# Kernel optimization log

Hardware: AMD Instinct MI355X
Metric: run time of the kernel (lower is better)

The kernel has to match this reference:

```python
import jax, jax.numpy as jnp
import numpy as np
from itertools import product


def _unnormalize(g, size, align_corners=True):
    # map [-1,1] -> pixel coords
    if align_corners:
        return (g + 1.0) * 0.5 * (size - 1)
    return ((g + 1.0) * size - 1.0) * 0.5


def grid_sample_4d(inp, grid, align_corners=True, padding_mode='zeros'):
    """inp: [N,C,X,Y,U,V], grid: [N,P,4] in [-1,1] -> out [N,C,P].
    16-corner quadrilinear interpolation."""
    N, C, X, Y, U, V = inp.shape
    sizes = (X, Y, U, V)
    coords = [_unnormalize(grid[..., d], sizes[d], align_corners) for d in range(4)]
    if padding_mode == 'border':
        coords = [jnp.clip(c, 0.0, sizes[d] - 1) for d, c in enumerate(coords)]
    lo = [jnp.floor(c) for c in coords]                     # [N,P] each
    frac = [c - l for c, l in zip(coords, lo)]
    lo_i = [l.astype(jnp.int32) for l in lo]
    inp_flat = inp.reshape(N, C, X * Y * U * V)
    out = jnp.zeros((N, C, grid.shape[1]), inp.dtype)
    for bits in product((0, 1), repeat=4):                  # 16 corners
        w = jnp.ones_like(frac[0])
        valid = jnp.ones(frac[0].shape, bool)
        idx = []
        for d in range(4):
            i = lo_i[d] + bits[d]
            w = w * (frac[d] if bits[d] else (1.0 - frac[d]))
            if padding_mode == 'zeros':
                valid = valid & (i >= 0) & (i < sizes[d])
            idx.append(jnp.clip(i, 0, sizes[d] - 1))
        if padding_mode == 'zeros':
            w = w * valid.astype(w.dtype)
        flat = ((idx[0] * Y + idx[1]) * U + idx[2]) * V + idx[3]   # [N,P]
        vals = jnp.take_along_axis(inp_flat, flat[:, None, :], axis=2)  # [N,C,P]
        out = out + w[:, None, :] * vals
    return out


def setup_inputs() -> dict:
    key = jax.random.key(0)
    k1, k2 = jax.random.split(key)
    N, C, X, Y, U, V = 1, 16, 8, 8, 256, 256
    P = 1_000_000
    inp = jax.random.normal(k1, (N, C, X, Y, U, V), dtype=jnp.float32)
    # slightly exceed [-1,1] to exercise zeros padding
    grid = jax.random.uniform(k2, (N, P, 4), dtype=jnp.float32, minval=-1.05, maxval=1.05)
    return {"input": inp, "grid": grid}


def reference(input, grid):
    return grid_sample_4d(input, grid, align_corners=True, padding_mode='zeros')
```

## Files before the change

### kernel.cpp

```cpp
#include <hip/hip_runtime.h>
#include <hip/hip_fp16.h>

namespace {
constexpr int CS = 16;
constexpr int XS = 8, YS = 8, US = 256, VS = 256;
constexpr int CH_STRIDE = XS * YS * US * VS;
constexpr size_t NVOX = (size_t)CH_STRIDE;
constexpr size_t TRANS_H_BYTES = NVOX * CS * 2;

__global__ __launch_bounds__(256) void transpose_h_kernel(
    const float* __restrict__ inp, __half* __restrict__ ws)
{
    __shared__ float lds[CS][257];
    size_t base = (size_t)blockIdx.x * 256;
    #pragma unroll
    for (int c = 0; c < CS; ++c)
        lds[c][threadIdx.x] = inp[(size_t)c * CH_STRIDE + base + threadIdx.x];
    __syncthreads();
    size_t obase = base * CS;
    #pragma unroll
    for (int it = 0; it < 2; ++it) {
        int flat0 = (it * 256 + threadIdx.x) * 8;
        uint4 pk;
        uint* pw = &pk.x;
        #pragma unroll
        for (int j = 0; j < 4; ++j) {
            int f0 = flat0 + j * 2, f1 = f0 + 1;
            __half2 h = __floats2half2_rn(lds[f0 & 15][f0 >> 4],
                                          lds[f1 & 15][f1 >> 4]);
            pw[j] = *reinterpret_cast<uint*>(&h);
        }
        *reinterpret_cast<uint4*>(ws + obase + flat0) = pk;
    }
}

__global__ __launch_bounds__(256) void gather_h_kernel(
    const __half* __restrict__ tin, const float* __restrict__ grid,
    float* __restrict__ out, int P)
{
    int p = blockIdx.x * 256 + threadIdx.x;
    if (p >= P) return;

    float4 g = reinterpret_cast<const float4*>(grid)[p];

    float c0 = (g.x + 1.0f) * 0.5f * (XS - 1);
    float c1 = (g.y + 1.0f) * 0.5f * (YS - 1);
    float c2 = (g.z + 1.0f) * 0.5f * (US - 1);
    float c3 = (g.w + 1.0f) * 0.5f * (VS - 1);

    float f0 = floorf(c0), f1 = floorf(c1), f2 = floorf(c2), f3 = floorf(c3);
    int i0 = (int)f0, i1 = (int)f1, i2 = (int)f2, i3 = (int)f3;
    float t0 = c0 - f0, t1 = c1 - f1, t2 = c2 - f2, t3 = c3 - f3;

    float w0[2], w1[2], w2[2], w3[2];
    int   q0[2], q1[2], q2[2], q3[2];
    #pragma unroll
    for (int b = 0; b < 2; ++b) {
        int j;
        j = i0 + b; w0[b] = (b ? t0 : 1.0f - t0) * ((j >= 0 && j < XS) ? 1.0f : 0.0f); q0[b] = min(max(j, 0), XS - 1);
        j = i1 + b; w1[b] = (b ? t1 : 1.0f - t1) * ((j >= 0 && j < YS) ? 1.0f : 0.0f); q1[b] = min(max(j, 0), YS - 1);
        j = i2 + b; w2[b] = (b ? t2 : 1.0f - t2) * ((j >= 0 && j < US) ? 1.0f : 0.0f); q2[b] = min(max(j, 0), US - 1);
        j = i3 + b; w3[b] = (b ? t3 : 1.0f - t3) * ((j >= 0 && j < VS) ? 1.0f : 0.0f); q3[b] = min(max(j, 0), VS - 1);
    }

    float a[16];
    #pragma unroll
    for (int i = 0; i < 16; ++i) a[i] = 0.0f;

    #pragma unroll
    for (int bx = 0; bx < 2; ++bx)
    #pragma unroll
    for (int by = 0; by < 2; ++by) {
        int   xy  = (q0[bx] * YS + q1[by]) << 16;
        float wxy = w0[bx] * w1[by];
        #pragma unroll
        for (int bu = 0; bu < 2; ++bu) {
            int   xyu  = xy + (q2[bu] << 8);
            float wxyu = wxy * w2[bu];
            #pragma unroll
            for (int bv = 0; bv < 2; ++bv) {
                int   vox = xyu + q3[bv];
                float w   = wxyu * w3[bv];
                const uint4* cp = reinterpret_cast<const uint4*>(tin) + (size_t)vox * 2;
                uint4 r0 = cp[0], r1 = cp[1];
                uint rr[8] = {r0.x, r0.y, r0.z, r0.w, r1.x, r1.y, r1.z, r1.w};
                #pragma unroll
                for (int j = 0; j < 8; ++j) {
                    float2 f = __half22float2(*reinterpret_cast<const __half2*>(&rr[j]));
                    a[2*j]     = fmaf(w, f.x, a[2*j]);
                    a[2*j + 1] = fmaf(w, f.y, a[2*j + 1]);
                }
            }
        }
    }

    #pragma unroll
    for (int c = 0; c < CS; ++c)
        __builtin_nontemporal_store(a[c], &out[(size_t)c * P + p]);
}

__global__ __launch_bounds__(256) void gs4d_fallback(
    const float* __restrict__ inp, const float* __restrict__ grid,
    float* __restrict__ out, int P)
{
    int p = blockIdx.x * 256 + threadIdx.x;
    if (p >= P) return;
    int c = blockIdx.y;
    float4 g = reinterpret_cast<const float4*>(grid)[p];
    float c0 = (g.x + 1.0f) * 0.5f * (XS - 1);
    float c1 = (g.y + 1.0f) * 0.5f * (YS - 1);
    float c2 = (g.z + 1.0f) * 0.5f * (US - 1);
    float c3 = (g.w + 1.0f) * 0.5f * (VS - 1);
    float f0 = floorf(c0), f1 = floorf(c1), f2 = floorf(c2), f3 = floorf(c3);
    int i0 = (int)f0, i1 = (int)f1, i2 = (int)f2, i3 = (int)f3;
    float t0 = c0 - f0, t1 = c1 - f1, t2 = c2 - f2, t3 = c3 - f3;
    float w0[2], w1[2], w2[2], w3[2];
    int   q0[2], q1[2], q2[2], q3[2];
    #pragma unroll
    for (int b = 0; b < 2; ++b) {
        int j;
        j = i0 + b; w0[b] = (b ? t0 : 1.0f - t0) * ((j >= 0 && j < XS) ? 1.0f : 0.0f); q0[b] = min(max(j, 0), XS - 1);
        j = i1 + b; w1[b] = (b ? t1 : 1.0f - t1) * ((j >= 0 && j < YS) ? 1.0f : 0.0f); q1[b] = min(max(j, 0), YS - 1);
        j = i2 + b; w2[b] = (b ? t2 : 1.0f - t2) * ((j >= 0 && j < US) ? 1.0f : 0.0f); q2[b] = min(max(j, 0), US - 1);
        j = i3 + b; w3[b] = (b ? t3 : 1.0f - t3) * ((j >= 0 && j < VS) ? 1.0f : 0.0f); q3[b] = min(max(j, 0), VS - 1);
    }
    const float* ip = inp + (size_t)c * CH_STRIDE;
    float acc = 0.0f;
    #pragma unroll
    for (int bx = 0; bx < 2; ++bx)
    #pragma unroll
    for (int by = 0; by < 2; ++by)
    #pragma unroll
    for (int bu = 0; bu < 2; ++bu)
    #pragma unroll
    for (int bv = 0; bv < 2; ++bv) {
        int idx = ((q0[bx] * YS + q1[by]) * US + q2[bu]) * VS + q3[bv];
        acc = fmaf(w0[bx] * w1[by] * w2[bu] * w3[bv], ip[idx], acc);
    }
    __builtin_nontemporal_store(acc, &out[(size_t)c * P + p]);
}
}

extern "C" void kernel_launch(void* const* d_in, const int* in_sizes, int n_in,
                              void* d_out, int out_size, void* d_ws, size_t ws_size,
                              hipStream_t stream) {
    const float* inp  = (const float*)d_in[0];
    const float* grid = (const float*)d_in[1];
    float* out = (float*)d_out;
    int P = in_sizes[1] / 4;
    int pblocks = (P + 255) / 256;

    if (ws_size >= TRANS_H_BYTES) {
        __half* ws = (__half*)d_ws;
        transpose_h_kernel<<<CH_STRIDE / 256, 256, 0, stream>>>(inp, ws);
        gather_h_kernel<<<pblocks, 256, 0, stream>>>(ws, grid, out, P);
    } else {
        dim3 blocks(pblocks, CS);
        gs4d_fallback<<<blocks, 256, 0, stream>>>(inp, grid, out, P);
    }
}
```

Baseline: 266.2 us.

## Add a second fp16 atlas shifted by one voxel to align v-neighbor pairs

The transpose kernel now writes two channel-interleaved fp16 copies of the input. The second copy is rotated by one voxel along V within each 256-voxel row. The gather kernel picks the copy by the parity of the lower V index, so the two V-neighbor voxels always start at an even slot and stay in one aligned 64-byte chunk, reducing cache-line crossings per gather. In exchange, the transpose writes twice as many bytes and the workspace footprint doubles, which may lower cache hit rates.

```diff
diff --git a/kernel.cpp b/kernel.cpp
--- a/kernel.cpp
+++ b/kernel.cpp
@@ -6,10 +6,12 @@
 constexpr int XS = 8, YS = 8, US = 256, VS = 256;
 constexpr int CH_STRIDE = XS * YS * US * VS;
 constexpr size_t NVOX = (size_t)CH_STRIDE;
-constexpr size_t TRANS_H_BYTES = NVOX * CS * 2;
-
-__global__ __launch_bounds__(256) void transpose_h_kernel(
-    const float* __restrict__ inp, __half* __restrict__ ws)
+constexpr size_t ATLAS_HALFS = NVOX * CS;
+constexpr size_t DUAL_BYTES  = ATLAS_HALFS * 2 * 2;
+constexpr size_t SINGLE_BYTES = ATLAS_HALFS * 2;
+
+__global__ __launch_bounds__(256) void transpose2_kernel(
+    const float* __restrict__ inp, __half* __restrict__ wsA, __half* __restrict__ wsB)
 {
     __shared__ float lds[CS][257];
     size_t base = (size_t)blockIdx.x * 256;
@@ -30,13 +32,14 @@
                                           lds[f1 & 15][f1 >> 4]);
             pw[j] = *reinterpret_cast<uint*>(&h);
         }
-        *reinterpret_cast<uint4*>(ws + obase + flat0) = pk;
-    }
-}
-
-__global__ __launch_bounds__(256) void gather_h_kernel(
-    const __half* __restrict__ tin, const float* __restrict__ grid,
-    float* __restrict__ out, int P)
+        *reinterpret_cast<uint4*>(wsA + obase + flat0) = pk;
+        *reinterpret_cast<uint4*>(wsB + obase + ((flat0 + 16) & 4095)) = pk;
+    }
+}
+
+__global__ __launch_bounds__(256) void gather_dual_kernel(
+    const __half* __restrict__ tinA, const __half* __restrict__ tinB,
+    const float* __restrict__ grid, float* __restrict__ out, int P)
 {
     int p = blockIdx.x * 256 + threadIdx.x;
     if (p >= P) return;
@@ -52,6 +55,99 @@
     int i0 = (int)f0, i1 = (int)f1, i2 = (int)f2, i3 = (int)f3;
     float t0 = c0 - f0, t1 = c1 - f1, t2 = c2 - f2, t3 = c3 - f3;
 
+    float w0[2], w1[2], w2[2], w3[2];
+    int   q0[2], q1[2], q2[2], slot3[2];
+    #pragma unroll
+    for (int b = 0; b < 2; ++b) {
+        int j;
+        j = i0 + b; w0[b] = (b ? t0 : 1.0f - t0) * ((j >= 0 && j < XS) ? 1.0f : 0.0f); q0[b] = min(max(j, 0), XS - 1);
+        j = i1 + b; w1[b] = (b ? t1 : 1.0f - t1) * ((j >= 0 && j < YS) ? 1.0f : 0.0f); q1[b] = min(max(j, 0), YS - 1);
+        j = i2 + b; w2[b] = (b ? t2 : 1.0f - t2) * ((j >= 0 && j < US) ? 1.0f : 0.0f); q2[b] = min(max(j, 0), US - 1);
+        j = i3 + b; w3[b] = (b ? t3 : 1.0f - t3) * ((j >= 0 && j < VS) ? 1.0f : 0.0f); slot3[b] = min(max(j, 0), VS - 1);
+    }
+    int parity = i3 & 1;
+    const __half* atlas = parity ? tinB : tinA;
+    if (parity) {
+        slot3[0] = (slot3[0] + 1) & 255;
+        slot3[1] = (slot3[1] + 1) & 255;
+    }
+
+    float a[16];
+    #pragma unroll
+    for (int i = 0; i < 16; ++i) a[i] = 0.0f;
+
+    #pragma unroll
+    for (int bx = 0; bx < 2; ++bx)
+    #pragma unroll
+    for (int by = 0; by < 2; ++by) {
+        int   xy  = (q0[bx] * YS + q1[by]) << 16;
+        float wxy = w0[bx] * w1[by];
+        #pragma unroll
+        for (int bu = 0; bu < 2; ++bu) {
+            int   xyu  = xy + (q2[bu] << 8);
+            float wxyu = wxy * w2[bu];
+            #pragma unroll
+            for (int bv = 0; bv < 2; ++bv) {
+                int   vox = xyu + slot3[bv];
+                float w   = wxyu * w3[bv];
+                const uint4* cp = reinterpret_cast<const uint4*>(atlas) + (size_t)vox * 2;
+                uint4 r0 = cp[0], r1 = cp[1];
+                uint rr[8] = {r0.x, r0.y, r0.z, r0.w, r1.x, r1.y, r1.z, r1.w};
+                #pragma unroll
+                for (int j = 0; j < 8; ++j) {
+                    float2 f = __half22float2(*reinterpret_cast<const __half2*>(&rr[j]));
+                    a[2*j]     = fmaf(w, f.x, a[2*j]);
+                    a[2*j + 1] = fmaf(w, f.y, a[2*j + 1]);
+                }
+            }
+        }
+    }
+
+    #pragma unroll
+    for (int c = 0; c < CS; ++c)
+        __builtin_nontemporal_store(a[c], &out[(size_t)c * P + p]);
+}
+
+__global__ __launch_bounds__(256) void transpose_h_kernel(
+    const float* __restrict__ inp, __half* __restrict__ ws)
+{
+    __shared__ float lds[CS][257];
+    size_t base = (size_t)blockIdx.x * 256;
+    #pragma unroll
+    for (int c = 0; c < CS; ++c)
+        lds[c][threadIdx.x] = inp[(size_t)c * CH_STRIDE + base + threadIdx.x];
+    __syncthreads();
+    size_t obase = base * CS;
+    #pragma unroll
+    for (int it = 0; it < 2; ++it) {
+        int flat0 = (it * 256 + threadIdx.x) * 8;
+        uint4 pk;
+        uint* pw = &pk.x;
+        #pragma unroll
+        for (int j = 0; j < 4; ++j) {
+            int f0 = flat0 + j * 2, f1 = f0 + 1;
+            __half2 h = __floats2half2_rn(lds[f0 & 15][f0 >> 4],
+                                          lds[f1 & 15][f1 >> 4]);
+            pw[j] = *reinterpret_cast<uint*>(&h);
+        }
+        *reinterpret_cast<uint4*>(ws + obase + flat0) = pk;
+    }
+}
+
+__global__ __launch_bounds__(256) void gather_h_kernel(
+    const __half* __restrict__ tin, const float* __restrict__ grid,
+    float* __restrict__ out, int P)
+{
+    int p = blockIdx.x * 256 + threadIdx.x;
+    if (p >= P) return;
+    float4 g = reinterpret_cast<const float4*>(grid)[p];
+    float c0 = (g.x + 1.0f) * 0.5f * (XS - 1);
+    float c1 = (g.y + 1.0f) * 0.5f * (YS - 1);
+    float c2 = (g.z + 1.0f) * 0.5f * (US - 1);
+    float c3 = (g.w + 1.0f) * 0.5f * (VS - 1);
+    float f0 = floorf(c0), f1 = floorf(c1), f2 = floorf(c2), f3 = floorf(c3);
+    int i0 = (int)f0, i1 = (int)f1, i2 = (int)f2, i3 = (int)f3;
+    float t0 = c0 - f0, t1 = c1 - f1, t2 = c2 - f2, t3 = c3 - f3;
     float w0[2], w1[2], w2[2], w3[2];
     int   q0[2], q1[2], q2[2], q3[2];
     #pragma unroll
@@ -62,11 +158,9 @@
         j = i2 + b; w2[b] = (b ? t2 : 1.0f - t2) * ((j >= 0 && j < US) ? 1.0f : 0.0f); q2[b] = min(max(j, 0), US - 1);
         j = i3 + b; w3[b] = (b ? t3 : 1.0f - t3) * ((j >= 0 && j < VS) ? 1.0f : 0.0f); q3[b] = min(max(j, 0), VS - 1);
     }
-
     float a[16];
     #pragma unroll
     for (int i = 0; i < 16; ++i) a[i] = 0.0f;
-
     #pragma unroll
     for (int bx = 0; bx < 2; ++bx)
     #pragma unroll
@@ -93,7 +187,6 @@
             }
         }
     }
-
     #pragma unroll
     for (int c = 0; c < CS; ++c)
         __builtin_nontemporal_store(a[c], &out[(size_t)c * P + p]);
@@ -150,7 +243,12 @@
     int P = in_sizes[1] / 4;
     int pblocks = (P + 255) / 256;
 
-    if (ws_size >= TRANS_H_BYTES) {
+    if (ws_size >= DUAL_BYTES) {
+        __half* wsA = (__half*)d_ws;
+        __half* wsB = wsA + ATLAS_HALFS;
+        transpose2_kernel<<<CH_STRIDE / 256, 256, 0, stream>>>(inp, wsA, wsB);
+        gather_dual_kernel<<<pblocks, 256, 0, stream>>>(wsA, wsB, grid, out, P);
+    } else if (ws_size >= SINGLE_BYTES) {
         __half* ws = (__half*)d_ws;
         transpose_h_kernel<<<CH_STRIDE / 256, 256, 0, stream>>>(inp, ws);
         gather_h_kernel<<<pblocks, 256, 0, stream>>>(ws, grid, out, P);
```

Result: slower. 284.6 us (+6.9%).

## Bucket grid points by U-slab to localize gathers in cache

Applied to the files above, without the earlier changes.

Adds a counting-sort pipeline: count points per U-range bucket, scan for offsets, scatter grid points into bucket order, run one gather pass per bucket into a workspace, then unpermute results into the output. The aim is for each gather pass to touch only about a quarter of the fp16 channel-last atlas (64 MB total), so that slab fits better in the last-level cache and random-gather DRAM traffic drops. In exchange it adds several extra kernel launches, a serial single-block scan, and extra global traffic for the sorted grid, the 64 MB intermediate result buffer and the inverse-permutation reads.

```diff
diff --git a/kernel.cpp b/kernel.cpp
--- a/kernel.cpp
+++ b/kernel.cpp
@@ -6,7 +6,10 @@
 constexpr int XS = 8, YS = 8, US = 256, VS = 256;
 constexpr int CH_STRIDE = XS * YS * US * VS;
 constexpr size_t NVOX = (size_t)CH_STRIDE;
-constexpr size_t TRANS_H_BYTES = NVOX * CS * 2;
+constexpr size_t ATLAS_HALFS = NVOX * CS;
+constexpr size_t SINGLE_BYTES = ATLAS_HALFS * 2;
+constexpr int NB = 4;
+constexpr int USH = 6;
 
 __global__ __launch_bounds__(256) void transpose_h_kernel(
     const float* __restrict__ inp, __half* __restrict__ ws)
@@ -34,24 +37,22 @@
     }
 }
 
-__global__ __launch_bounds__(256) void gather_h_kernel(
-    const __half* __restrict__ tin, const float* __restrict__ grid,
-    float* __restrict__ out, int P)
-{
-    int p = blockIdx.x * 256 + threadIdx.x;
-    if (p >= P) return;
-
-    float4 g = reinterpret_cast<const float4*>(grid)[p];
-
+__device__ __forceinline__ int bucket_of(const float4& g) {
+    float c2 = (g.z + 1.0f) * 0.5f * (US - 1);
+    int iu = min(max((int)floorf(c2), 0), US - 1);
+    return iu >> USH;
+}
+
+__device__ __forceinline__ void gather_point(
+    const __half* __restrict__ tin, const float4& g, float* a)
+{
     float c0 = (g.x + 1.0f) * 0.5f * (XS - 1);
     float c1 = (g.y + 1.0f) * 0.5f * (YS - 1);
     float c2 = (g.z + 1.0f) * 0.5f * (US - 1);
     float c3 = (g.w + 1.0f) * 0.5f * (VS - 1);
-
     float f0 = floorf(c0), f1 = floorf(c1), f2 = floorf(c2), f3 = floorf(c3);
     int i0 = (int)f0, i1 = (int)f1, i2 = (int)f2, i3 = (int)f3;
     float t0 = c0 - f0, t1 = c1 - f1, t2 = c2 - f2, t3 = c3 - f3;
-
     float w0[2], w1[2], w2[2], w3[2];
     int   q0[2], q1[2], q2[2], q3[2];
     #pragma unroll
@@ -62,11 +63,8 @@
         j = i2 + b; w2[b] = (b ? t2 : 1.0f - t2) * ((j >= 0 && j < US) ? 1.0f : 0.0f); q2[b] = min(max(j, 0), US - 1);
         j = i3 + b; w3[b] = (b ? t3 : 1.0f - t3) * ((j >= 0 && j < VS) ? 1.0f : 0.0f); q3[b] = min(max(j, 0), VS - 1);
     }
-
-    float a[16];
     #pragma unroll
     for (int i = 0; i < 16; ++i) a[i] = 0.0f;
-
     #pragma unroll
     for (int bx = 0; bx < 2; ++bx)
     #pragma unroll
@@ -93,7 +91,127 @@
             }
         }
     }
-
+}
+
+__global__ __launch_bounds__(256) void blockcount_kernel(
+    const float* __restrict__ grid, int* __restrict__ bc, int P)
+{
+    __shared__ int cnt[NB];
+    if (threadIdx.x < NB) cnt[threadIdx.x] = 0;
+    __syncthreads();
+    int p = blockIdx.x * 256 + threadIdx.x;
+    if (p < P) {
+        float4 g = reinterpret_cast<const float4*>(grid)[p];
+        atomicAdd(&cnt[bucket_of(g)], 1);
+    }
+    __syncthreads();
+    if (threadIdx.x < NB) bc[blockIdx.x * NB + threadIdx.x] = cnt[threadIdx.x];
+}
+
+__global__ __launch_bounds__(256) void scan_kernel(
+    const int* __restrict__ bc, int* __restrict__ base, int* __restrict__ off, int T)
+{
+    __shared__ int part[256][NB];
+    __shared__ int boff[NB + 1];
+    int t = threadIdx.x;
+    int chunk = (T + 255) / 256;
+    int s[NB];
+    #pragma unroll
+    for (int b = 0; b < NB; ++b) s[b] = 0;
+    for (int i = 0; i < chunk; ++i) {
+        int blk = t * chunk + i;
+        if (blk < T)
+            #pragma unroll
+            for (int b = 0; b < NB; ++b) s[b] += bc[blk * NB + b];
+    }
+    #pragma unroll
+    for (int b = 0; b < NB; ++b) part[t][b] = s[b];
+    __syncthreads();
+    for (int o = 1; o < 256; o <<= 1) {
+        int v[NB];
+        #pragma unroll
+        for (int b = 0; b < NB; ++b) v[b] = (t >= o) ? part[t - o][b] : 0;
+        __syncthreads();
+        #pragma unroll
+        for (int b = 0; b < NB; ++b) part[t][b] += v[b];
+        __syncthreads();
+    }
+    if (t == 0) {
+        boff[0] = 0;
+        for (int b = 0; b < NB; ++b) boff[b + 1] = boff[b] + part[255][b];
+        for (int b = 0; b <= NB; ++b) off[b] = boff[b];
+    }
+    __syncthreads();
+    int run[NB];
+    #pragma unroll
+    for (int b = 0; b < NB; ++b) run[b] = boff[b] + part[t][b] - s[b];
+    for (int i = 0; i < chunk; ++i) {
+        int blk = t * chunk + i;
+        if (blk < T)
+            #pragma unroll
+            for (int b = 0; b < NB; ++b) { base[blk * NB + b] = run[b]; run[b] += bc[blk * NB + b]; }
+    }
+}
+
+__global__ __launch_bounds__(256) void scatter_kernel(
+    const float* __restrict__ grid, const int* __restrict__ base,
+    float4* __restrict__ sg, int* __restrict__ inv, int P)
+{
+    __shared__ int rank[NB];
+    if (threadIdx.x < NB) rank[threadIdx.x] = 0;
+    __syncthreads();
+    int p = blockIdx.x * 256 + threadIdx.x;
+    if (p >= P) return;
+    float4 g = reinterpret_cast<const float4*>(grid)[p];
+    int b = bucket_of(g);
+    int r = atomicAdd(&rank[b], 1);
+    int s = base[blockIdx.x * NB + b] + r;
+    sg[s] = g;
+    inv[p] = s;
+}
+
+__global__ __launch_bounds__(256) void gather_bucket_kernel(
+    const __half* __restrict__ tin, const float4* __restrict__ sg,
+    float4* __restrict__ ws2, const int* __restrict__ off, int k)
+{
+    int lo = off[k], hi = off[k + 1];
+    for (int s = lo + blockIdx.x * 256 + threadIdx.x; s < hi; s += gridDim.x * 256) {
+        float4 g = sg[s];
+        float a[16];
+        gather_point(tin, g, a);
+        float4* d = ws2 + (size_t)s * 4;
+        d[0] = make_float4(a[0], a[1], a[2], a[3]);
+        d[1] = make_float4(a[4], a[5], a[6], a[7]);
+        d[2] = make_float4(a[8], a[9], a[10], a[11]);
+        d[3] = make_float4(a[12], a[13], a[14], a[15]);
+    }
+}
+
+__global__ __launch_bounds__(256) void unpermute_kernel(
+    const float4* __restrict__ ws2, const int* __restrict__ inv,
+    float* __restrict__ out, int P)
+{
+    int p = blockIdx.x * 256 + threadIdx.x;
+    if (p >= P) return;
+    int s = inv[p];
+    const float4* src = ws2 + (size_t)s * 4;
+    float4 r0 = src[0], r1 = src[1], r2 = src[2], r3 = src[3];
+    float r[16] = {r0.x,r0.y,r0.z,r0.w, r1.x,r1.y,r1.z,r1.w,
+                   r2.x,r2.y,r2.z,r2.w, r3.x,r3.y,r3.z,r3.w};
+    #pragma unroll
+    for (int c = 0; c < CS; ++c)
+        __builtin_nontemporal_store(r[c], &out[(size_t)c * P + p]);
+}
+
+__global__ __launch_bounds__(256) void gather_h_kernel(
+    const __half* __restrict__ tin, const float* __restrict__ grid,
+    float* __restrict__ out, int P)
+{
+    int p = blockIdx.x * 256 + threadIdx.x;
+    if (p >= P) return;
+    float4 g = reinterpret_cast<const float4*>(grid)[p];
+    float a[16];
+    gather_point(tin, g, a);
     #pragma unroll
     for (int c = 0; c < CS; ++c)
         __builtin_nontemporal_store(a[c], &out[(size_t)c * P + p]);
@@ -150,7 +268,32 @@
     int P = in_sizes[1] / 4;
     int pblocks = (P + 255) / 256;
 
-    if (ws_size >= TRANS_H_BYTES) {
+    size_t f_atlas  = ATLAS_HALFS / 2;
+    size_t f_sorted = (size_t)P * 4;
+    size_t f_ws2    = (size_t)P * 16;
+    size_t f_inv    = (size_t)P;
+    size_t f_bc     = (size_t)pblocks * NB;
+    size_t f_base   = (size_t)pblocks * NB;
+    size_t need = (f_atlas + f_sorted + f_ws2 + f_inv + f_bc + f_base + NB + 8) * 4;
+
+    if (ws_size >= need) {
+        __half* atlas      = (__half*)d_ws;
+        float*  ws0        = (float*)d_ws;
+        float4* sortedgrid = (float4*)(ws0 + f_atlas);
+        float4* ws2        = (float4*)(ws0 + f_atlas + f_sorted);
+        int*    inv        = (int*)  (ws0 + f_atlas + f_sorted + f_ws2);
+        int*    bc         = inv + f_inv;
+        int*    base       = bc + f_bc;
+        int*    off        = base + f_base;
+
+        transpose_h_kernel<<<CH_STRIDE / 256, 256, 0, stream>>>(inp, atlas);
+        blockcount_kernel<<<pblocks, 256, 0, stream>>>(grid, bc, P);
+        scan_kernel<<<1, 256, 0, stream>>>(bc, base, off, pblocks);
+        scatter_kernel<<<pblocks, 256, 0, stream>>>(grid, base, sortedgrid, inv, P);
+        for (int k = 0; k < NB; ++k)
+            gather_bucket_kernel<<<1024, 256, 0, stream>>>(atlas, sortedgrid, ws2, off, k);
+        unpermute_kernel<<<pblocks, 256, 0, stream>>>(ws2, inv, out, P);
+    } else if (ws_size >= SINGLE_BYTES) {
         __half* ws = (__half*)d_ws;
         transpose_h_kernel<<<CH_STRIDE / 256, 256, 0, stream>>>(inp, ws);
         gather_h_kernel<<<pblocks, 256, 0, stream>>>(ws, grid, out, P);
```

Result: slower. 383.2 us (+44.0%).
